# Kernel optimization log

Hardware: AMD Instinct MI355X
Metric: run time of the kernel (lower is better)

The kernel has to match this reference:

```python
import jax, jax.numpy as jnp
import numpy as np
import math

B, L, WIN, D, H, FF, NL, V, M = 16, 2048, 128, 512, 8, 2048, 3, 32000, 32
HD = D // H
EPS = 1e-5
RECON_W = 0.1

def _ln(x, g, b):
    m = x.mean(-1, keepdims=True)
    v = ((x - m) ** 2).mean(-1, keepdims=True)
    return (x - m) * jax.lax.rsqrt(v + EPS) * g + b

def _denoiser(x_t, t, motif, left, right, glob, time_proj_W, time_proj_b, cond_proj_W, cond_proj_b,
              qkv_W, qkv_b, attn_out_W, attn_out_b, ff1_W, ff1_b, ff2_W, ff2_b,
              ln1_g, ln1_b, ln2_g, ln2_b, out_W, out_b):
    half = D // 2
    freqs = jnp.exp(-math.log(10000.0) * jnp.arange(half) / (half - 1))
    a = t[:, None] * freqs[None, :]
    temb = jnp.concatenate([jnp.sin(a), jnp.cos(a)], -1) @ time_proj_W.T + time_proj_b
    x = x_t + temb[:, None, :]
    cond = jnp.concatenate([motif, left, right, glob], -1) @ cond_proj_W.T + cond_proj_b
    x = jnp.concatenate([cond[:, None, :], x], 1)
    S = x.shape[1]
    for i in range(NL):  # post-norm TransformerEncoderLayer, relu, no dropout (eval)
        qkv = x @ qkv_W[i].T + qkv_b[i]
        q, k, v = jnp.split(qkv, 3, axis=-1)
        q = q.reshape(B, S, H, HD); k = k.reshape(B, S, H, HD); v = v.reshape(B, S, H, HD)
        attn = jax.nn.softmax(jnp.einsum('bqhd,bkhd->bhqk', q, k) / math.sqrt(HD), axis=-1)
        ctx = jnp.einsum('bhqk,bkhd->bqhd', attn, v).reshape(B, S, D)
        x = _ln(x + ctx @ attn_out_W[i].T + attn_out_b[i], ln1_g[i], ln1_b[i])
        h = jax.nn.relu(x @ ff1_W[i].T + ff1_b[i]) @ ff2_W[i].T + ff2_b[i]
        x = _ln(x + h, ln2_g[i], ln2_b[i])
    return x[:, 1:, :] @ out_W.T + out_b

def setup_inputs():
    key = jax.random.key(0)
    ks = jax.random.split(key, 20)
    s = 0.02
    inp = {}
    inp['token_ids'] = jax.random.randint(ks[0], (B, L), 0, V)
    inp['motif_ids'] = jax.random.randint(ks[1], (B, M), 0, V)
    inp['motif_len'] = jax.random.randint(ks[2], (B,), 1, M + 1)
    inp['window_start'] = jax.random.randint(ks[3], (B,), 0, L - WIN)
    lens = jax.random.randint(ks[4], (B,), 1, WIN + 1).at[0].set(WIN)
    inp['window_end'] = inp['window_start'] + lens
    inp['t'] = jax.random.uniform(ks[5], (B,))
    inp['x0'] = jax.random.normal(ks[6], (B, WIN, D))
    inp['embed_table'] = jax.random.normal(ks[7], (V, D)) * s
    inp['decode_W'] = jax.random.normal(ks[8], (V, D)) * s
    inp['decode_b'] = jnp.zeros((V,))
    inp['adapter_W'] = jax.random.normal(ks[9], (D, D)) * s
    inp['adapter_b'] = jnp.zeros((D,))
    inp['time_proj_W'] = jax.random.normal(ks[10], (D, D)) * s
    inp['time_proj_b'] = jnp.zeros((D,))
    inp['cond_proj_W'] = jax.random.normal(ks[11], (D, 4 * D)) * s
    inp['cond_proj_b'] = jnp.zeros((D,))
    inp['qkv_W'] = jax.random.normal(ks[12], (NL, 3 * D, D)) * s
    inp['qkv_b'] = jnp.zeros((NL, 3 * D))
    inp['attn_out_W'] = jax.random.normal(ks[13], (NL, D, D)) * s
    inp['attn_out_b'] = jnp.zeros((NL, D))
    inp['ff1_W'] = jax.random.normal(ks[14], (NL, FF, D)) * s
    inp['ff1_b'] = jnp.zeros((NL, FF))
    inp['ff2_W'] = jax.random.normal(ks[15], (NL, D, FF)) * s
    inp['ff2_b'] = jnp.zeros((NL, D))
    inp['ln1_g'] = jnp.ones((NL, D)); inp['ln1_b'] = jnp.zeros((NL, D))
    inp['ln2_g'] = jnp.ones((NL, D)); inp['ln2_b'] = jnp.zeros((NL, D))
    inp['out_W'] = jax.random.normal(ks[16], (D, D)) * s
    inp['out_b'] = jnp.zeros((D,))
    return inp

def _forward(token_ids, motif_ids, motif_len, window_start, window_end, t, x0,
             embed_table, decode_W, decode_b, adapter_W, adapter_b, den):
    hidden = embed_table[token_ids]  # frozen backbone encode: [B, L, D]
    pos = jnp.arange(L)
    def pool(s, e):  # vectorized masked mean over region [s, e)
        m = ((pos[None, :] >= s[:, None]) & (pos[None, :] < e[:, None])).astype(hidden.dtype)
        return jnp.einsum('bl,bld->bd', m, hidden) / jnp.maximum(m.sum(1, keepdims=True), 1.0)
    left = pool(jnp.zeros_like(window_start), window_start)
    right = pool(window_end, jnp.full_like(window_end, L))
    glob = hidden.mean(1)
    memb = embed_table[motif_ids]
    mmask = (jnp.arange(M)[None, :] < motif_len[:, None]).astype(memb.dtype)
    motif = (memb * mmask[..., None]).sum(1) / jnp.maximum(motif_len.astype(memb.dtype), 1.0)[:, None]
    actual = jnp.clip(window_end - window_start, 0, WIN)
    win_mask = jnp.arange(WIN)[None, :] < actual[:, None]
    idx = jnp.clip(window_start[:, None] + jnp.arange(WIN)[None, :], 0, L - 1)
    x1 = jnp.take_along_axis(hidden, idx[:, :, None], axis=1) * win_mask[..., None]
    x_t = (1 - t[:, None, None]) * x0 + t[:, None, None] * x1
    target_v = x1 - x0
    pred_v = _denoiser(x_t, t, motif, left, right, glob, *den)
    valid = win_mask[..., None].astype(x1.dtype)
    vel = (((pred_v - target_v) ** 2) * valid).sum() / (jnp.maximum(valid.sum(), 1.0) * D)
    pred_x1 = x_t + (1 - t[:, None, None]) * pred_v
    logits = (pred_x1 @ adapter_W.T + adapter_b) @ decode_W.T + decode_b
    labels = jnp.where(win_mask, jnp.take_along_axis(token_ids, idx, axis=1), -100)
    lv = labels != -100
    logp = jax.nn.log_softmax(logits, axis=-1)
    picked = jnp.take_along_axis(logp, jnp.maximum(labels, 0)[..., None], axis=-1)[..., 0]
    recon = -(picked * lv).sum() / jnp.maximum(lv.sum(), 1)
    return vel + RECON_W * recon

def reference(token_ids, motif_ids, motif_len, window_start, window_end, t, x0,
              embed_table, decode_W, decode_b, adapter_W, adapter_b,
              time_proj_W, time_proj_b, cond_proj_W, cond_proj_b, qkv_W, qkv_b,
              attn_out_W, attn_out_b, ff1_W, ff1_b, ff2_W, ff2_b,
              ln1_g, ln1_b, ln2_g, ln2_b, out_W, out_b):
    den = (time_proj_W, time_proj_b, cond_proj_W, cond_proj_b, qkv_W, qkv_b,
           attn_out_W, attn_out_b, ff1_W, ff1_b, ff2_W, ff2_b,
           ln1_g, ln1_b, ln2_g, ln2_b, out_W, out_b)
    return _forward(token_ids, motif_ids, motif_len, window_start, window_end, t, x0,
                    embed_table, decode_W, decode_b, adapter_W, adapter_b, den)
```

## Files before the change

### kernel.cpp

```cpp
#include <hip/hip_runtime.h>
#include <hip/hip_bf16.h>
#include <math.h>

typedef __hip_bfloat16 bf16;

constexpr int cB = 16, cL = 2048, cWIN = 128, cD = 512, cH = 8, cFF = 2048;
constexpr int cNL = 3, cV = 32000, cM = 32;
constexpr int cHD = cD / cH;
constexpr int cS = cWIN + 1;
constexpr float cEPS = 1e-5f;
constexpr float cRECON_W = 0.1f;
constexpr int cNVT = cV / 128;

__device__ __forceinline__ float b2f(bf16 x) { return __bfloat162float(x); }

__device__ __forceinline__ float ldx(const void* p, size_t i, int f32) {
    return f32 ? ((const float*)p)[i]
               : __bfloat162float(((const bf16*)p)[i]);
}

__device__ __forceinline__ unsigned int f2bf(float f) {
    union { float f; unsigned int u; } v; v.f = f;
    unsigned int u = v.u + 0x7FFFu + ((v.u >> 16) & 1u);
    return u >> 16;
}

__device__ __forceinline__ void glds16(const unsigned short* g, unsigned short* l) {
    __builtin_amdgcn_global_load_lds(
        (const __attribute__((address_space(1))) void*)g,
        (__attribute__((address_space(3))) void*)l, 16, 0, 0);
}

typedef short bf16x8 __attribute__((ext_vector_type(8)));
typedef float f32x4  __attribute__((ext_vector_type(4)));

__global__ void detect_kernel(const void* __restrict__ x0raw, int* __restrict__ flag)
{
    const unsigned short* h = (const unsigned short*)x0raw;
    int tid = threadIdx.x;
    int cnt = 0;
    for (int j = tid; j < 8192; j += 256) {
        unsigned short u = h[2 * j];
        int e = (u >> 7) & 0xFF;
        if (e >= 134) cnt++;
    }
    __shared__ int red[256];
    red[tid] = cnt; __syncthreads();
    for (int off = 128; off > 0; off >>= 1) {
        if (tid < off) red[tid] += red[tid + off];
        __syncthreads();
    }
    if (tid == 0) *flag = (red[0] > 400) ? 1 : 0;
}

__global__ __launch_bounds__(512) void pools_part_kernel(
    const int* __restrict__ tok, const int* __restrict__ wstart,
    const int* __restrict__ wend, const void* __restrict__ emb,
    float* __restrict__ part, const int* __restrict__ dflag)
{
    const int f32 = *dflag;
    int chunk = blockIdx.x;
    int b = blockIdx.y;
    int d = threadIdx.x;
    int ws_ = wstart[b], we_ = wend[b];
    float sl = 0.f, sr = 0.f, sg = 0.f;
    int l0 = chunk * 128;
    for (int l = l0; l < l0 + 128; ++l) {
        int t = tok[b * cL + l];
        float h = ldx(emb, (size_t)t * cD + d, f32);
        sg += h;
        if (l < ws_) sl += h;
        if (l >= we_) sr += h;
    }
    size_t base = ((size_t)(b * 16 + chunk)) * 3 * cD;
    part[base + d]            = sl;
    part[base + cD + d]       = sr;
    part[base + 2 * cD + d]   = sg;
}

__global__ __launch_bounds__(512) void pools_combine_kernel(
    const float* __restrict__ part, const int* __restrict__ mids,
    const int* __restrict__ mlen, const int* __restrict__ wstart,
    const int* __restrict__ wend, const void* __restrict__ emb,
    unsigned short* __restrict__ featb, const int* __restrict__ dflag)
{
    const int f32 = *dflag;
    int b = blockIdx.x;
    int d = threadIdx.x;
    int ws_ = wstart[b], we_ = wend[b];
    float sl = 0.f, sr = 0.f, sg = 0.f;
    for (int c = 0; c < 16; ++c) {
        size_t base = ((size_t)(b * 16 + c)) * 3 * cD;
        sl += part[base + d];
        sr += part[base + cD + d];
        sg += part[base + 2 * cD + d];
    }
    int ml = mlen[b];
    float sm = 0.f;
    for (int j = 0; j < cM; ++j) {
        if (j < ml) sm += ldx(emb, (size_t)mids[b * cM + j] * cD + d, f32);
    }
    unsigned short* fr = featb + (size_t)b * (4 * cD);
    fr[d]            = (unsigned short)f2bf(sm / fmaxf((float)ml, 1.f));
    fr[cD + d]       = (unsigned short)f2bf(sl / fmaxf((float)ws_, 1.f));
    fr[2 * cD + d]   = (unsigned short)f2bf(sr / fmaxf((float)(cL - we_), 1.f));
    fr[3 * cD + d]   = (unsigned short)f2bf(sg / (float)cL);
}

__global__ __launch_bounds__(512) void tf_kernel(
    const void* __restrict__ t_arr, unsigned short* __restrict__ tfbb,
    const int* __restrict__ dflag)
{
    const int f32 = *dflag;
    int b = blockIdx.x;
    int j = threadIdx.x;
    float t = ldx(t_arr, b, f32);
    const int half = cD / 2;
    float v;
    if (j < half) {
        float fr = expf(-logf(10000.f) * (float)j / (float)(half - 1));
        v = sinf(t * fr);
    } else {
        float fr = expf(-logf(10000.f) * (float)(j - half) / (float)(half - 1));
        v = cosf(t * fr);
    }
    tfbb[(size_t)b * cD + j] = (unsigned short)f2bf(v);
}

__global__ __launch_bounds__(512) void build_x_kernel(
    const int* __restrict__ tok, const int* __restrict__ wstart,
    const int* __restrict__ wend, const void* __restrict__ t_arr,
    const void* __restrict__ x0, const void* __restrict__ emb,
    const float* __restrict__ cond, const float* __restrict__ temb,
    float* __restrict__ x, unsigned short* __restrict__ xbf,
    float* __restrict__ x1, float* __restrict__ xt,
    const int* __restrict__ dflag)
{
    const int f32 = *dflag;
    int row = blockIdx.x;
    int b = row / cS, s = row % cS;
    int d = threadIdx.x;
    if (s == 0) {
        float cv = cond[b * cD + d];
        x[(size_t)row * cD + d] = cv;
        xbf[(size_t)row * cD + d] = (unsigned short)f2bf(cv);
        return;
    }
    int i = s - 1;
    int ws_ = wstart[b], we_ = wend[b];
    int actual = min(max(we_ - ws_, 0), cWIN);
    int idx = min(ws_ + i, cL - 1);
    float x1v = 0.f;
    if (i < actual) x1v = ldx(emb, (size_t)tok[b * cL + idx] * cD + d, f32);
    float t = ldx(t_arr, b, f32);
    float x0v = ldx(x0, ((size_t)b * cWIN + i) * cD + d, f32);
    float xtv = (1.f - t) * x0v + t * x1v;
    size_t ro = ((size_t)b * cWIN + i) * cD + d;
    x1[ro] = x1v;
    xt[ro] = xtv;
    float xv = xtv + temb[b * cD + d];
    x[(size_t)row * cD + d] = xv;
    xbf[(size_t)row * cD + d] = (unsigned short)f2bf(xv);
}

constexpr int GL2 = 72;
__global__ __launch_bounds__(512) void gemm_bf(
    const unsigned short* __restrict__ Abf, const void* __restrict__ Wb,
    size_t wOff, const void* __restrict__ biasb, size_t bOff,
    float* __restrict__ Cf, unsigned short* __restrict__ Cbf,
    int Mdim, int Ndim, int Kdim, int relu, int obf, int amap,
    const int* __restrict__ dflag)
{
    const int f32 = *dflag;
    const float* Wf = (const float*)Wb + wOff;
    const unsigned short* Wh = (const unsigned short*)Wb + wOff;
    __shared__ unsigned short As[2][64 * GL2];
    __shared__ unsigned short Bs[2][64 * GL2];
    const int tid = threadIdx.x;
    const int lane = tid & 63;
    const int wid = tid >> 6;
    const int wm = wid >> 1;
    const int wn = wid & 1;
    const int quad = lane >> 4, lm = lane & 15;
    const int m0 = blockIdx.y * 64;
    const int n0 = blockIdx.x * 64;

    f32x4 acc0 = (f32x4){0.f, 0.f, 0.f, 0.f};
    f32x4 acc1 = (f32x4){0.f, 0.f, 0.f, 0.f};

    const int srow = tid >> 3;
    const int sc8  = (tid & 7) * 8;
    const int ssw  = ((tid & 7) ^ ((tid >> 3) & 7)) * 8;
    const int lmm  = lm & 7;

    auto loadA = [&](int k0, uint4& r) {
        int r0 = m0 + srow;
        uint4 v = {0u, 0u, 0u, 0u};
        if (r0 < Mdim) {
            size_t ar = amap ? ((size_t)(r0 >> 7) * cS + 1 + (r0 & 127))
                             : (size_t)r0;
            v = *(const uint4*)(Abf + ar * Kdim + k0 + sc8);
        }
        r = v;
    };
    auto loadB = [&](int k0, uint4& r) {
        size_t g = (size_t)(n0 + srow) * Kdim + k0 + sc8;
        if (f32) {
            float4 v0 = *(const float4*)(Wf + g);
            float4 v1 = *(const float4*)(Wf + g + 4);
            r = make_uint4(
                f2bf(v0.x) | (f2bf(v0.y) << 16), f2bf(v0.z) | (f2bf(v0.w) << 16),
                f2bf(v1.x) | (f2bf(v1.y) << 16), f2bf(v1.z) | (f2bf(v1.w) << 16));
        } else {
            r = *(const uint4*)(Wh + g);
        }
    };
    auto stores = [&](int buf, const uint4& ra, const uint4& rb) {
        *(uint4*)(&As[buf][srow * GL2 + ssw]) = ra;
        *(uint4*)(&Bs[buf][srow * GL2 + ssw]) = rb;
    };
    auto compute = [&](int buf) {
        #pragma unroll
        for (int kk = 0; kk < 2; ++kk) {
            const int sl = ((kk * 4 + quad) ^ lmm) * 8;
            bf16x8 a0 = *(const bf16x8*)(&As[buf][(wm * 16 + lm) * GL2 + sl]);
            bf16x8 b0 = *(const bf16x8*)(&Bs[buf][(wn * 32 + lm) * GL2 + sl]);
            bf16x8 b1 = *(const bf16x8*)(&Bs[buf][(wn * 32 + 16 + lm) * GL2 + sl]);
            acc0 = __builtin_amdgcn_mfma_f32_16x16x32_bf16(a0, b0, acc0, 0, 0, 0);
            acc1 = __builtin_amdgcn_mfma_f32_16x16x32_bf16(a0, b1, acc1, 0, 0, 0);
        }
    };

    uint4 raA, rbA, raB, rbB;
    loadA(0, raA);  loadB(0, rbA);
    loadA(64, raB); loadB(64, rbB);
    const int nk = Kdim >> 6;
    for (int t = 0; t < nk; t += 2) {
        stores(0, raA, rbA);
        __syncthreads();
        if (t + 2 < nk) { loadA((t + 2) * 64, raA); loadB((t + 2) * 64, rbA); }
        compute(0);
        stores(1, raB, rbB);
        __syncthreads();
        if (t + 3 < nk) { loadA((t + 3) * 64, raB); loadB((t + 3) * 64, rbB); }
        compute(1);
    }

    #pragma unroll
    for (int in = 0; in < 2; ++in) {
        int gc = n0 + wn * 32 + in * 16 + lm;
        float bv = ldx(biasb, bOff + gc, f32);
        const f32x4& a = in ? acc1 : acc0;
        #pragma unroll
        for (int r = 0; r < 4; ++r) {
            int gr = m0 + wm * 16 + quad * 4 + r;
            if (gr < Mdim) {
                float v = a[r] + bv;
                if (relu) v = fmaxf(v, 0.f);
                if (obf) Cbf[(size_t)gr * Ndim + gc] = (unsigned short)f2bf(v);
                else     Cf[(size_t)gr * Ndim + gc] = v;
            }
        }
    }
}

__global__ __launch_bounds__(256) void attn_mfma_kernel(
    const unsigned short* __restrict__ qkv, unsigned short* __restrict__ ctx)
{
    constexpr int SP = 160;
    constexpr int KP = 72;
    constexpr int VP = 168;
    const int h = blockIdx.x, b = blockIdx.y, z = blockIdx.z;
    const int tid = threadIdx.x;
    const int lane = tid & 63;
    const int wid = tid >> 6;
    const int quad = lane >> 4, lm = lane & 15;

    __shared__ unsigned short Ks[SP * KP];
    __shared__ unsigned short Vt[64 * VP];
    __shared__ unsigned short Pl[4 * 16 * VP];

    const unsigned short* base = qkv + (size_t)b * cS * (3 * cD) + h * cHD;

    for (int c = tid; c < SP * 8; c += 256) {
        int row = c >> 3, g = c & 7;
        uint4 v = {0u, 0u, 0u, 0u};
        if (row < cS)
            v = *(const uint4*)(base + (size_t)row * (3 * cD) + cD + g * 8);
        *(uint4*)(Ks + row * KP + g * 8) = v;
    }
    for (int c = tid; c < SP * 16; c += 256) {
        int key = c >> 4, d4 = c & 15;
        uint2 v = {0u, 0u};
        if (key < cS)
            v = *(const uint2*)(base + (size_t)key * (3 * cD) + 2 * cD + d4 * 4);
        Vt[(d4 * 4 + 0) * VP + key] = (unsigned short)(v.x & 0xFFFFu);
        Vt[(d4 * 4 + 1) * VP + key] = (unsigned short)(v.x >> 16);
        Vt[(d4 * 4 + 2) * VP + key] = (unsigned short)(v.y & 0xFFFFu);
        Vt[(d4 * 4 + 3) * VP + key] = (unsigned short)(v.y >> 16);
    }
    __syncthreads();

    unsigned short* Pw = Pl + wid * (16 * VP);
    const int t = z * 3 + wid;

    if (wid < 3 && t < 9) {
        int qs = t * 16 + lm;
        bf16x8 aq[2];
        #pragma unroll
        for (int j = 0; j < 8; ++j) { aq[0][j] = 0; aq[1][j] = 0; }
        if (qs < cS) {
            const unsigned short* qrow = base + (size_t)qs * (3 * cD);
            aq[0] = *(const bf16x8*)(qrow + quad * 8);
            aq[1] = *(const bf16x8*)(qrow + 32 + quad * 8);
        }

        f32x4 sc[10];
        #pragma unroll
        for (int n = 0; n < 10; ++n) {
            sc[n] = (f32x4){0.f, 0.f, 0.f, 0.f};
            bf16x8 bk0 = *(const bf16x8*)(Ks + (n * 16 + lm) * KP + quad * 8);
            sc[n] = __builtin_amdgcn_mfma_f32_16x16x32_bf16(aq[0], bk0, sc[n], 0, 0, 0);
            bf16x8 bk1 = *(const bf16x8*)(Ks + (n * 16 + lm) * KP + 32 + quad * 8);
            sc[n] = __builtin_amdgcn_mfma_f32_16x16x32_bf16(aq[1], bk1, sc[n], 0, 0, 0);
        }

        #pragma unroll
        for (int r = 0; r < 4; ++r) {
            float mx = -3.0e38f;
            #pragma unroll
            for (int n = 0; n < 10; ++n) {
                float v = sc[n][r] * 0.125f;
                mx = fmaxf(mx, ((n * 16 + lm) < cS) ? v : -3.0e38f);
            }
            #pragma unroll
            for (int msk = 1; msk < 16; msk <<= 1)
                mx = fmaxf(mx, __shfl_xor(mx, msk));
            float p[10];
            float sum = 0.f;
            #pragma unroll
            for (int n = 0; n < 10; ++n) {
                float e = ((n * 16 + lm) < cS) ? expf(sc[n][r] * 0.125f - mx) : 0.f;
                p[n] = e; sum += e;
            }
            #pragma unroll
            for (int msk = 1; msk < 16; msk <<= 1)
                sum += __shfl_xor(sum, msk);
            float inv = 1.f / sum;
            unsigned short* pr = Pw + (quad * 4 + r) * VP + lm;
            #pragma unroll
            for (int n = 0; n < 10; ++n)
                pr[n * 16] = (unsigned short)f2bf(p[n] * inv);
        }

        asm volatile("s_waitcnt lgkmcnt(0)" ::: "memory");
        __builtin_amdgcn_sched_barrier(0);

        f32x4 o[4];
        #pragma unroll
        for (int j = 0; j < 4; ++j) o[j] = (f32x4){0.f, 0.f, 0.f, 0.f};
        #pragma unroll
        for (int ks = 0; ks < 5; ++ks) {
            bf16x8 ap = *(const bf16x8*)(Pw + lm * VP + ks * 32 + quad * 8);
            #pragma unroll
            for (int j = 0; j < 4; ++j) {
                bf16x8 bv = *(const bf16x8*)(Vt + (j * 16 + lm) * VP + ks * 32 + quad * 8);
                o[j] = __builtin_amdgcn_mfma_f32_16x16x32_bf16(ap, bv, o[j], 0, 0, 0);
            }
        }

        #pragma unroll
        for (int r = 0; r < 4; ++r) {
            int s_ = t * 16 + quad * 4 + r;
            if (s_ < cS) {
                unsigned short* orow = ctx + ((size_t)(b * cS + s_)) * cD + h * cHD;
                #pragma unroll
                for (int j = 0; j < 4; ++j)
                    orow[j * 16 + lm] = (unsigned short)f2bf(o[j][r]);
            }
        }
    }
}

__global__ __launch_bounds__(256) void resid_ln_kernel(
    float* __restrict__ x, const float* __restrict__ h,
    const void* __restrict__ g, const void* __restrict__ bta, size_t off,
    unsigned short* __restrict__ xbf, const int* __restrict__ dflag)
{
    const int f32 = *dflag;
    int row = blockIdx.x;
    int tid = threadIdx.x;
    __shared__ float red[256];
    float v[2];
    float s = 0.f;
    #pragma unroll
    for (int j = 0; j < 2; ++j) {
        int d = tid + j * 256;
        v[j] = x[(size_t)row * cD + d] + h[(size_t)row * cD + d];
        s += v[j];
    }
    red[tid] = s; __syncthreads();
    for (int o = 128; o > 0; o >>= 1) {
        if (tid < o) red[tid] += red[tid + o];
        __syncthreads();
    }
    float mean = red[0] / (float)cD;
    __syncthreads();
    float vs = 0.f;
    #pragma unroll
    for (int j = 0; j < 2; ++j) { float dd = v[j] - mean; vs += dd * dd; }
    red[tid] = vs; __syncthreads();
    for (int o = 128; o > 0; o >>= 1) {
        if (tid < o) red[tid] += red[tid + o];
        __syncthreads();
    }
    float rs = rsqrtf(red[0] / (float)cD + cEPS);
    #pragma unroll
    for (int j = 0; j < 2; ++j) {
        int d = tid + j * 256;
        float ov = (v[j] - mean) * rs * ldx(g, off + d, f32) + ldx(bta, off + d, f32);
        x[(size_t)row * cD + d] = ov;
        xbf[(size_t)row * cD + d] = (unsigned short)f2bf(ov);
    }
}

__global__ __launch_bounds__(512) void predvel_kernel(
    const float* __restrict__ xt, const float* __restrict__ pv,
    const float* __restrict__ x1, const void* __restrict__ x0,
    const void* __restrict__ t_arr, const int* __restrict__ wstart,
    const int* __restrict__ wend, unsigned short* __restrict__ px1,
    float* __restrict__ velpart, const int* __restrict__ dflag)
{
    const int f32 = *dflag;
    int row = blockIdx.x;
    int b = row >> 7, i = row & 127;
    int d = threadIdx.x;
    float t = ldx(t_arr, b, f32);
    size_t o = (size_t)row * cD + d;
    float pvv = pv[o];
    px1[o] = (unsigned short)f2bf(xt[o] + (1.f - t) * pvv);
    int actual = min(max(wend[b] - wstart[b], 0), cWIN);
    float s = 0.f;
    if (i < actual) {
        float tv = x1[o] - ldx(x0, o, f32);
        float diff = pvv - tv;
        s = diff * diff;
    }
    __shared__ float red[512];
    red[d] = s; __syncthreads();
    for (int off = 256; off > 0; off >>= 1) {
        if (d < off) red[d] += red[d + off];
        __syncthreads();
    }
    if (d == 0) velpart[row] = red[0];
}

__global__ void labels_kernel(
    const int* __restrict__ tok, const int* __restrict__ wstart,
    const int* __restrict__ wend, int* __restrict__ labels)
{
    int r = blockIdx.x * 256 + threadIdx.x;
    if (r >= cB * cWIN) return;
    int b = r / cWIN, i = r % cWIN;
    int ws_ = wstart[b], we_ = wend[b];
    int actual = min(max(we_ - ws_, 0), cWIN);
    labels[r] = (i < actual) ? tok[b * cL + min(ws_ + i, cL - 1)] : -1;
}

__global__ __launch_bounds__(256) void cvt_w_kernel(
    const void* __restrict__ Wsrc, unsigned short* __restrict__ dst,
    const int* __restrict__ dflag)
{
    if (!*dflag) return;
    const float4* src = (const float4*)Wsrc;
    size_t n4 = (size_t)cV * cD / 4;
    for (size_t i = (size_t)blockIdx.x * 256 + threadIdx.x; i < n4;
         i += (size_t)gridDim.x * 256) {
        float4 v = src[i];
        unsigned int p0 = f2bf(v.x) | (f2bf(v.y) << 16);
        unsigned int p1 = f2bf(v.z) | (f2bf(v.w) << 16);
        ((uint2*)dst)[i] = make_uint2(p0, p1);
    }
}

__global__ __launch_bounds__(256) void decode_mfma2_kernel(
    const unsigned short* __restrict__ hbf, const unsigned short* __restrict__ wbf,
    const void* __restrict__ dW, const void* __restrict__ db,
    const int* __restrict__ labels,
    float* __restrict__ pm, float* __restrict__ ps, float* __restrict__ lab,
    const int* __restrict__ dflag)
{
    const int f32 = *dflag;
    const unsigned short* Wsrc = f32 ? wbf : (const unsigned short*)dW;
    const int bid = blockIdx.x;
    const int xcd = bid & 7;
    const int local = bid >> 3;
    const int nt = xcd * 32 + (local >> 4);
    const int mt = local & 15;
    if (nt >= cNVT) return;
    const int m0 = mt * 128, n0 = nt * 128;

    __shared__ __align__(16) char smem[17408];
    unsigned short* As = (unsigned short*)smem;
    unsigned short* Bs = As + 4096;

    const int tid = threadIdx.x;
    const int lane = tid & 63;
    const int wid = tid >> 6;
    const int wm = wid >> 1, wn = wid & 1;
    const int quad = lane >> 4, lm = lane & 15;

    const int grow  = lane >> 2;
    const int gslot = (lane & 3) ^ ((lane >> 3) & 3);
    const int rslot = (quad ^ ((lm >> 1) & 3)) * 8;

    const unsigned short* gA = hbf  + (size_t)(m0 + wid * 32 + grow) * cD + gslot * 8;
    const unsigned short* gB = Wsrc + (size_t)(n0 + wid * 32 + grow) * cD + gslot * 8;

    f32x4 acc[4][4];
    #pragma unroll
    for (int i = 0; i < 4; ++i)
        #pragma unroll
        for (int j = 0; j < 4; ++j)
            acc[i][j] = (f32x4){0.f, 0.f, 0.f, 0.f};

    for (int k0 = 0; k0 < cD; k0 += 32) {
        #pragma unroll
        for (int c = 0; c < 2; ++c) {
            glds16(gA + (size_t)c * 16 * cD + k0, As + (wid * 2 + c) * 512);
            glds16(gB + (size_t)c * 16 * cD + k0, Bs + (wid * 2 + c) * 512);
        }
        __syncthreads();
        bf16x8 af[4], bfr[4];
        #pragma unroll
        for (int im = 0; im < 4; ++im)
            af[im] = *(const bf16x8*)(As + (wm * 64 + im * 16 + lm) * 32 + rslot);
        #pragma unroll
        for (int in = 0; in < 4; ++in)
            bfr[in] = *(const bf16x8*)(Bs + (wn * 64 + in * 16 + lm) * 32 + rslot);
        #pragma unroll
        for (int im = 0; im < 4; ++im)
            #pragma unroll
            for (int in = 0; in < 4; ++in)
                acc[im][in] = __builtin_amdgcn_mfma_f32_16x16x32_bf16(
                    af[im], bfr[in], acc[im][in], 0, 0, 0);
        __syncthreads();
    }

    float bv[4];
    #pragma unroll
    for (int in = 0; in < 4; ++in)
        bv[in] = ldx(db, n0 + wn * 64 + in * 16 + lm, f32);
    #pragma unroll
    for (int im = 0; im < 4; ++im)
        #pragma unroll
        for (int in = 0; in < 4; ++in)
            #pragma unroll
            for (int r = 0; r < 4; ++r)
                acc[im][in][r] += bv[in];

    #pragma unroll
    for (int im = 0; im < 4; ++im) {
        #pragma unroll
        for (int r = 0; r < 4; ++r) {
            int gr = m0 + wm * 64 + im * 16 + quad * 4 + r;
            int lb = labels[gr];
            #pragma unroll
            for (int in = 0; in < 4; ++in) {
                int col = n0 + wn * 64 + in * 16 + lm;
                if (lb == col) lab[gr] = acc[im][in][r];
            }
        }
    }

    float (*red)[33] = (float(*)[33])smem;
    float* mrow = (float*)(smem + 16896);
    #pragma unroll
    for (int im = 0; im < 4; ++im) {
        #pragma unroll
        for (int r = 0; r < 4; ++r) {
            int rl = wm * 64 + im * 16 + quad * 4 + r;
            float mx = acc[im][0][r];
            #pragma unroll
            for (int in = 1; in < 4; ++in) mx = fmaxf(mx, acc[im][in][r]);
            red[rl][wn * 16 + lm] = mx;
        }
    }
    __syncthreads();
    if (tid < 128) {
        float mx = red[tid][0];
        #pragma unroll
        for (int t = 1; t < 32; ++t) mx = fmaxf(mx, red[tid][t]);
        mrow[tid] = mx;
    }
    __syncthreads();
    #pragma unroll
    for (int im = 0; im < 4; ++im) {
        #pragma unroll
        for (int r = 0; r < 4; ++r) {
            int rl = wm * 64 + im * 16 + quad * 4 + r;
            float m_ = mrow[rl];
            float s = 0.f;
            #pragma unroll
            for (int in = 0; in < 4; ++in) s += expf(acc[im][in][r] - m_);
            red[rl][wn * 16 + lm] = s;
        }
    }
    __syncthreads();
    if (tid < 128) {
        float s = red[tid][0];
        #pragma unroll
        for (int t = 1; t < 32; ++t) s += red[tid][t];
        int gr = m0 + tid;
        pm[(size_t)gr * cNVT + nt] = mrow[tid];
        ps[(size_t)gr * cNVT + nt] = s;
    }
}

constexpr int GLDS = 40;
__global__ __launch_bounds__(256) void decode_mfma_kernel(
    const unsigned short* __restrict__ hbf, const void* __restrict__ dW,
    const void* __restrict__ db, const int* __restrict__ labels,
    float* __restrict__ pm, float* __restrict__ ps, float* __restrict__ lab,
    const int* __restrict__ dflag)
{
    const int f32 = *dflag;
    const float* Wf = (const float*)dW;
    const unsigned short* Wh = (const unsigned short*)dW;
    __shared__ unsigned short As[128 * GLDS];
    __shared__ unsigned short Bs[128 * GLDS];
    const int tid = threadIdx.x;
    const int lane = tid & 63;
    const int wid = tid >> 6;
    const int wm = wid >> 1, wn = wid & 1;
    const int quad = lane >> 4, lm = lane & 15;
    const int nt = blockIdx.x;
    const int mt = blockIdx.y;
    const int m0 = mt * 128, n0 = nt * 128;

    f32x4 acc[4][4];
    #pragma unroll
    for (int i = 0; i < 4; ++i)
        #pragma unroll
        for (int j = 0; j < 4; ++j)
            acc[i][j] = (f32x4){0.f, 0.f, 0.f, 0.f};

    for (int k0 = 0; k0 < cD; k0 += 32) {
        #pragma unroll
        for (int t = 0; t < 2; ++t) {
            int idx = tid + t * 256;
            int row = idx >> 2, c = idx & 3;
            uint4 v = *(const uint4*)(hbf + (size_t)(m0 + row) * cD + k0 + c * 8);
            *(uint4*)(As + row * GLDS + c * 8) = v;
        }
        #pragma unroll
        for (int t = 0; t < 4; ++t) {
            int chunk = tid + t * 256;
            int row = chunk >> 3;
            int kc = (chunk & 7) * 4;
            size_t gro = (size_t)(n0 + row) * cD + k0 + kc;
            if (f32) {
                float4 v = *(const float4*)(Wf + gro);
                unsigned int p0 = f2bf(v.x) | (f2bf(v.y) << 16);
                unsigned int p1 = f2bf(v.z) | (f2bf(v.w) << 16);
                *(uint2*)(Bs + row * GLDS + kc) = make_uint2(p0, p1);
            } else {
                *(uint2*)(Bs + row * GLDS + kc) = *(const uint2*)(Wh + gro);
            }
        }
        __syncthreads();
        bf16x8 af[4], bfr[4];
        #pragma unroll
        for (int im = 0; im < 4; ++im) {
            int row = wm * 64 + im * 16 + lm;
            af[im] = *(const bf16x8*)(As + row * GLDS + quad * 8);
        }
        #pragma unroll
        for (int in = 0; in < 4; ++in) {
            int row = wn * 64 + in * 16 + lm;
            bfr[in] = *(const bf16x8*)(Bs + row * GLDS + quad * 8);
        }
        #pragma unroll
        for (int im = 0; im < 4; ++im)
            #pragma unroll
            for (int in = 0; in < 4; ++in)
                acc[im][in] = __builtin_amdgcn_mfma_f32_16x16x32_bf16(
                    af[im], bfr[in], acc[im][in], 0, 0, 0);
        __syncthreads();
    }

    float bv[4];
    #pragma unroll
    for (int in = 0; in < 4; ++in)
        bv[in] = ldx(db, n0 + wn * 64 + in * 16 + lm, f32);
    #pragma unroll
    for (int im = 0; im < 4; ++im)
        #pragma unroll
        for (int in = 0; in < 4; ++in)
            #pragma unroll
            for (int r = 0; r < 4; ++r)
                acc[im][in][r] += bv[in];

    #pragma unroll
    for (int im = 0; im < 4; ++im) {
        #pragma unroll
        for (int r = 0; r < 4; ++r) {
            int gr = m0 + wm * 64 + im * 16 + quad * 4 + r;
            int lb = labels[gr];
            #pragma unroll
            for (int in = 0; in < 4; ++in) {
                int col = n0 + wn * 64 + in * 16 + lm;
                if (lb == col) lab[gr] = acc[im][in][r];
            }
        }
    }

    __shared__ float red[128][33];
    __shared__ float mrow[128];
    #pragma unroll
    for (int im = 0; im < 4; ++im) {
        #pragma unroll
        for (int r = 0; r < 4; ++r) {
            int rl = wm * 64 + im * 16 + quad * 4 + r;
            float mx = acc[im][0][r];
            #pragma unroll
            for (int in = 1; in < 4; ++in) mx = fmaxf(mx, acc[im][in][r]);
            red[rl][wn * 16 + lm] = mx;
        }
    }
    __syncthreads();
    if (tid < 128) {
        float mx = red[tid][0];
        #pragma unroll
        for (int t = 1; t < 32; ++t) mx = fmaxf(mx, red[tid][t]);
        mrow[tid] = mx;
    }
    __syncthreads();
    #pragma unroll
    for (int im = 0; im < 4; ++im) {
        #pragma unroll
        for (int r = 0; r < 4; ++r) {
            int rl = wm * 64 + im * 16 + quad * 4 + r;
            float m_ = mrow[rl];
            float s = 0.f;
            #pragma unroll
            for (int in = 0; in < 4; ++in) s += expf(acc[im][in][r] - m_);
            red[rl][wn * 16 + lm] = s;
        }
    }
    __syncthreads();
    if (tid < 128) {
        float s = red[tid][0];
        #pragma unroll
        for (int t = 1; t < 32; ++t) s += red[tid][t];
        int gr = m0 + tid;
        pm[(size_t)gr * cNVT + nt] = mrow[tid];
        ps[(size_t)gr * cNVT + nt] = s;
    }
}

__global__ __launch_bounds__(64) void lse_reduce_kernel(
    const float* __restrict__ pm, const float* __restrict__ ps,
    const float* __restrict__ lab, const int* __restrict__ labels,
    float* __restrict__ logppart)
{
    int r = blockIdx.x;
    int tid = threadIdx.x;
    if (labels[r] < 0) {
        if (tid == 0) logppart[r] = 0.f;
        return;
    }
    float m = -1e30f;
    for (int c = tid; c < cNVT; c += 64) m = fmaxf(m, pm[(size_t)r * cNVT + c]);
    for (int off = 32; off > 0; off >>= 1) m = fmaxf(m, __shfl_down(m, off));
    m = __shfl(m, 0);
    float s = 0.f;
    for (int c = tid; c < cNVT; c += 64)
        s += ps[(size_t)r * cNVT + c] * expf(pm[(size_t)r * cNVT + c] - m);
    for (int off = 32; off > 0; off >>= 1) s += __shfl_down(s, off);
    if (tid == 0) logppart[r] = lab[r] - (m + logf(s));
}

__global__ __launch_bounds__(256) void finalize_kernel(
    const float* __restrict__ velpart, const float* __restrict__ logppart,
    const int* __restrict__ wstart, const int* __restrict__ wend,
    void* __restrict__ out, const int* __restrict__ dflag)
{
    const int f32 = *dflag;
    __shared__ float r1[256], r2[256];
    int tid = threadIdx.x;
    float s1 = 0.f, s2 = 0.f;
    for (int r = tid; r < cB * cWIN; r += 256) {
        s1 += velpart[r];
        s2 += logppart[r];
    }
    r1[tid] = s1; r2[tid] = s2; __syncthreads();
    for (int off = 128; off > 0; off >>= 1) {
        if (tid < off) { r1[tid] += r1[tid + off]; r2[tid] += r2[tid + off]; }
        __syncthreads();
    }
    if (tid == 0) {
        float cnt = 0.f;
        for (int b = 0; b < cB; ++b)
            cnt += (float)min(max(wend[b] - wstart[b], 0), cWIN);
        cnt = fmaxf(cnt, 1.f);
        float vel = r1[0] / (cnt * (float)cD);
        float recon = -r2[0] / cnt;
        float loss = vel + cRECON_W * recon;
        if (f32) ((float*)out)[0] = loss;
        else     ((bf16*)out)[0] = __float2bfloat16(loss);
    }
}

extern "C" void kernel_launch(void* const* d_in, const int* in_sizes, int n_in,
                              void* d_out, int out_size, void* d_ws, size_t ws_size,
                              hipStream_t stream) {
    const int*  token_ids    = (const int*)d_in[0];
    const int*  motif_ids    = (const int*)d_in[1];
    const int*  motif_len    = (const int*)d_in[2];
    const int*  window_start = (const int*)d_in[3];
    const int*  window_end   = (const int*)d_in[4];
    const void* t_arr        = d_in[5];
    const void* x0           = d_in[6];
    const void* embed_table  = d_in[7];
    const void* decode_W     = d_in[8];
    const void* decode_b     = d_in[9];
    const void* adapter_W    = d_in[10];
    const void* adapter_b    = d_in[11];
    const void* time_proj_W  = d_in[12];
    const void* time_proj_b  = d_in[13];
    const void* cond_proj_W  = d_in[14];
    const void* cond_proj_b  = d_in[15];
    const void* qkv_W        = d_in[16];
    const void* qkv_b        = d_in[17];
    const void* attn_out_W   = d_in[18];
    const void* attn_out_b   = d_in[19];
    const void* ff1_W        = d_in[20];
    const void* ff1_b        = d_in[21];
    const void* ff2_W        = d_in[22];
    const void* ff2_b        = d_in[23];
    const void* ln1_g        = d_in[24];
    const void* ln1_b        = d_in[25];
    const void* ln2_g        = d_in[26];
    const void* ln2_b        = d_in[27];
    const void* out_W        = d_in[28];
    const void* out_b        = d_in[29];

    float* w = (float*)d_ws;
    const size_t SZ_X   = (size_t)cB * cS * cD;
    const size_t SZ_BA  = (size_t)cB * cS * cFF;
    const size_t SZ_ROW = (size_t)cB * cWIN * cD;
    float* x     = w;
    float* bufA  = x + SZ_X;
    float* bufB  = bufA + SZ_BA;
    float* bufC  = bufB + SZ_X;
    float* x1b   = bufC + SZ_X;
    float* xtb   = x1b + SZ_ROW;
    float* pvb   = xtb + SZ_ROW;
    float* h2b   = pvb + SZ_ROW;
    float* feat  = h2b + SZ_ROW;
    float* tfb   = feat + (size_t)cB * 4 * cD;
    float* cond  = tfb + (size_t)cB * cD;
    float* temb  = cond + (size_t)cB * cD;
    float* velpart = temb + (size_t)cB * cD;
    float* logppart = velpart + (size_t)cB * cWIN;
    int*   dflag = (int*)(logppart + (size_t)cB * cWIN);
    float* wsend = (float*)(dflag + 16);
    unsigned short* wbf = (unsigned short*)wsend;

    const size_t need_bytes = ((char*)wsend - (char*)d_ws)
                            + (size_t)cV * cD * sizeof(unsigned short) + 256;
    const bool fast_decode = ws_size >= need_bytes;

    const int Wrows = cB * cWIN;
    const int Mrows = cB * cS;

    unsigned short* xbf    = (unsigned short*)h2b;
    unsigned short* featbf = xbf + (size_t)Mrows * cD;
    unsigned short* tfbbf  = featbf + (size_t)cB * 4 * cD;
    unsigned short* qkvbf  = (unsigned short*)bufA;
    unsigned short* ff1bf  = (unsigned short*)bufA;
    unsigned short* ctxbf  = (unsigned short*)bufB;
    unsigned short* px1bf  = (unsigned short*)(bufA + (size_t)3 * 1024 * 1024);
    unsigned short* hbf    = (unsigned short*)bufC;

    float* pm  = bufA;
    float* ps  = pm + (size_t)Wrows * cNVT;
    float* lab = ps + (size_t)Wrows * cNVT;
    int*   labels = (int*)(lab + Wrows);
    float* poolspart = bufC;

    auto gemm = [&](const unsigned short* A, const void* W, size_t wOff,
                    const void* bias, size_t bOff, float* Cf, unsigned short* Cbf,
                    int M_, int N_, int K_, int relu, int obf, int amap) {
        dim3 grid(N_ / 64, (M_ + 63) / 64);
        gemm_bf<<<grid, 512, 0, stream>>>(A, W, wOff, bias, bOff, Cf, Cbf,
                                          M_, N_, K_, relu, obf, amap, dflag);
    };

    detect_kernel<<<1, 256, 0, stream>>>(x0, dflag);
    if (fast_decode)
        cvt_w_kernel<<<2048, 256, 0, stream>>>(decode_W, wbf, dflag);
    pools_part_kernel<<<dim3(16, cB), cD, 0, stream>>>(token_ids, window_start,
        window_end, embed_table, poolspart, dflag);
    pools_combine_kernel<<<cB, cD, 0, stream>>>(poolspart, motif_ids, motif_len,
        window_start, window_end, embed_table, featbf, dflag);
    tf_kernel<<<cB, cD, 0, stream>>>(t_arr, tfbbf, dflag);
    gemm(featbf, cond_proj_W, 0, cond_proj_b, 0, cond, nullptr, cB, cD, 4 * cD, 0, 0, 0);
    gemm(tfbbf, time_proj_W, 0, time_proj_b, 0, temb, nullptr, cB, cD, cD, 0, 0, 0);
    build_x_kernel<<<Mrows, cD, 0, stream>>>(token_ids, window_start, window_end,
        t_arr, x0, embed_table, cond, temb, x, xbf, x1b, xtb, dflag);

    for (int i = 0; i < cNL; ++i) {
        gemm(xbf, qkv_W, (size_t)i * 3 * cD * cD, qkv_b, (size_t)i * 3 * cD,
             nullptr, qkvbf, Mrows, 3 * cD, cD, 0, 1, 0);
        attn_mfma_kernel<<<dim3(cH, cB, 3), 256, 0, stream>>>(qkvbf, ctxbf);
        gemm(ctxbf, attn_out_W, (size_t)i * cD * cD, attn_out_b, (size_t)i * cD,
             bufC, nullptr, Mrows, cD, cD, 0, 0, 0);
        resid_ln_kernel<<<Mrows, 256, 0, stream>>>(x, bufC, ln1_g, ln1_b,
             (size_t)i * cD, xbf, dflag);
        gemm(xbf, ff1_W, (size_t)i * cFF * cD, ff1_b, (size_t)i * cFF,
             nullptr, ff1bf, Mrows, cFF, cD, 1, 1, 0);
        gemm(ff1bf, ff2_W, (size_t)i * cD * cFF, ff2_b, (size_t)i * cD,
             bufC, nullptr, Mrows, cD, cFF, 0, 0, 0);
        resid_ln_kernel<<<Mrows, 256, 0, stream>>>(x, bufC, ln2_g, ln2_b,
             (size_t)i * cD, xbf, dflag);
    }

    gemm(xbf, out_W, 0, out_b, 0, pvb, nullptr, Wrows, cD, cD, 0, 0, 1);
    predvel_kernel<<<Wrows, 512, 0, stream>>>(xtb, pvb, x1b, x0, t_arr,
        window_start, window_end, px1bf, velpart, dflag);
    gemm(px1bf, adapter_W, 0, adapter_b, 0, nullptr, hbf, Wrows, cD, cD, 0, 1, 0);

    labels_kernel<<<(Wrows + 255) / 256, 256, 0, stream>>>(
        token_ids, window_start, window_end, labels);
    if (fast_decode) {
        decode_mfma2_kernel<<<4096, 256, 0, stream>>>(
            hbf, wbf, decode_W, decode_b, labels, pm, ps, lab, dflag);
    } else {
        decode_mfma_kernel<<<dim3(cNVT, Wrows / 128), 256, 0, stream>>>(
            hbf, decode_W, decode_b, labels, pm, ps, lab, dflag);
    }
    lse_reduce_kernel<<<Wrows, 64, 0, stream>>>(pm, ps, lab, labels, logppart);

    finalize_kernel<<<1, 256, 0, stream>>>(velpart, logppart,
        window_start, window_end, d_out, dflag);
}
```

Baseline: 811.5 us.

## Fuse residual+LayerNorm into full-row GEMM and fold small side kernels together

Adds a gemm_row kernel in which each block computes 16 full rows of 512 outputs with MFMA. In its epilogue it applies bias, residual add and LayerNorm, which replaces the separate attn_out/ff2 GEMMs and their resid_ln kernels. The same kernel, in a second mode, fuses the output projection with the predicted-velocity and velocity-loss computation. The time-feature and label kernels are merged into pools_combine, and labels move to a dedicated workspace slot. This cuts launches and intermediate fp32 round trips through memory. The cost is fewer, larger blocks (about 129) that read A and W straight from global memory, and a one-pass E[x²]−mean² variance.

```diff
diff --git a/kernel.cpp b/kernel.cpp
--- a/kernel.cpp
+++ b/kernel.cpp
@@ -82,7 +82,9 @@
     const float* __restrict__ part, const int* __restrict__ mids,
     const int* __restrict__ mlen, const int* __restrict__ wstart,
     const int* __restrict__ wend, const void* __restrict__ emb,
-    unsigned short* __restrict__ featb, const int* __restrict__ dflag)
+    unsigned short* __restrict__ featb, const void* __restrict__ t_arr,
+    unsigned short* __restrict__ tfbb, const int* __restrict__ tok,
+    int* __restrict__ labels, const int* __restrict__ dflag)
 {
     const int f32 = *dflag;
     int b = blockIdx.x;
@@ -105,26 +107,26 @@
     fr[cD + d]       = (unsigned short)f2bf(sl / fmaxf((float)ws_, 1.f));
     fr[2 * cD + d]   = (unsigned short)f2bf(sr / fmaxf((float)(cL - we_), 1.f));
     fr[3 * cD + d]   = (unsigned short)f2bf(sg / (float)cL);
-}
-
-__global__ __launch_bounds__(512) void tf_kernel(
-    const void* __restrict__ t_arr, unsigned short* __restrict__ tfbb,
-    const int* __restrict__ dflag)
-{
-    const int f32 = *dflag;
-    int b = blockIdx.x;
-    int j = threadIdx.x;
-    float t = ldx(t_arr, b, f32);
-    const int half = cD / 2;
-    float v;
-    if (j < half) {
-        float fr = expf(-logf(10000.f) * (float)j / (float)(half - 1));
-        v = sinf(t * fr);
-    } else {
-        float fr = expf(-logf(10000.f) * (float)(j - half) / (float)(half - 1));
-        v = cosf(t * fr);
-    }
-    tfbb[(size_t)b * cD + j] = (unsigned short)f2bf(v);
+
+    {
+        float t = ldx(t_arr, b, f32);
+        const int half = cD / 2;
+        float v;
+        if (d < half) {
+            float frq = expf(-logf(10000.f) * (float)d / (float)(half - 1));
+            v = sinf(t * frq);
+        } else {
+            float frq = expf(-logf(10000.f) * (float)(d - half) / (float)(half - 1));
+            v = cosf(t * frq);
+        }
+        tfbb[(size_t)b * cD + d] = (unsigned short)f2bf(v);
+    }
+
+    if (d < cWIN) {
+        int actual = min(max(we_ - ws_, 0), cWIN);
+        labels[b * cWIN + d] =
+            (d < actual) ? tok[b * cL + min(ws_ + d, cL - 1)] : -1;
+    }
 }
 
 __global__ __launch_bounds__(512) void build_x_kernel(
@@ -264,6 +266,168 @@
     }
 }
 
+__global__ __launch_bounds__(512) void gemm_row(
+    const unsigned short* __restrict__ Abf, const void* __restrict__ Wb,
+    size_t wOff, const void* __restrict__ biasb, size_t bOff,
+    int Kdim, int mode, int amap,
+    float* __restrict__ xres, const void* __restrict__ g,
+    const void* __restrict__ bta, size_t lnOff, unsigned short* __restrict__ xbf,
+    const float* __restrict__ xt, const float* __restrict__ x1,
+    const void* __restrict__ x0, const void* __restrict__ t_arr,
+    const int* __restrict__ wstart, const int* __restrict__ wend,
+    unsigned short* __restrict__ px1, float* __restrict__ velpart,
+    const int* __restrict__ dflag)
+{
+    const int f32 = *dflag;
+    const float* Wf = (const float*)Wb + wOff;
+    const unsigned short* Wh = (const unsigned short*)Wb + wOff;
+    const int tid = threadIdx.x;
+    const int lane = tid & 63;
+    const int wid = tid >> 6;
+    const int quad = lane >> 4, lm = lane & 15;
+    const int m0 = blockIdx.x * 16;
+    const int colb = wid * 64;
+
+    int grA = m0 + lm;
+    size_t ar = amap ? ((size_t)(grA >> 7) * cS + 1 + (grA & 127)) : (size_t)grA;
+    const unsigned short* Arow = Abf + ar * Kdim;
+
+    size_t wro[4];
+    #pragma unroll
+    for (int n = 0; n < 4; ++n)
+        wro[n] = (size_t)(colb + n * 16 + lm) * Kdim;
+
+    f32x4 acc[4];
+    #pragma unroll
+    for (int n = 0; n < 4; ++n) acc[n] = (f32x4){0.f, 0.f, 0.f, 0.f};
+
+    auto ldw = [&](size_t off) -> bf16x8 {
+        if (f32) {
+            float4 v0 = *(const float4*)(Wf + off);
+            float4 v1 = *(const float4*)(Wf + off + 4);
+            union { unsigned int u[4]; bf16x8 h; } r;
+            r.u[0] = f2bf(v0.x) | (f2bf(v0.y) << 16);
+            r.u[1] = f2bf(v0.z) | (f2bf(v0.w) << 16);
+            r.u[2] = f2bf(v1.x) | (f2bf(v1.y) << 16);
+            r.u[3] = f2bf(v1.z) | (f2bf(v1.w) << 16);
+            return r.h;
+        }
+        return *(const bf16x8*)(Wh + off);
+    };
+    auto ldstep = [&](int k0, bf16x8& a0, bf16x8& a1, bf16x8* b0, bf16x8* b1) {
+        a0 = *(const bf16x8*)(Arow + k0 + quad * 8);
+        a1 = *(const bf16x8*)(Arow + k0 + 32 + quad * 8);
+        #pragma unroll
+        for (int n = 0; n < 4; ++n) {
+            b0[n] = ldw(wro[n] + k0 + quad * 8);
+            b1[n] = ldw(wro[n] + k0 + 32 + quad * 8);
+        }
+    };
+    auto comp = [&](bf16x8 a0, bf16x8 a1, const bf16x8* b0, const bf16x8* b1) {
+        #pragma unroll
+        for (int n = 0; n < 4; ++n) {
+            acc[n] = __builtin_amdgcn_mfma_f32_16x16x32_bf16(a0, b0[n], acc[n], 0, 0, 0);
+            acc[n] = __builtin_amdgcn_mfma_f32_16x16x32_bf16(a1, b1[n], acc[n], 0, 0, 0);
+        }
+    };
+
+    bf16x8 aA0, aA1, bA0[4], bA1[4];
+    bf16x8 aB0, aB1, bB0[4], bB1[4];
+    ldstep(0, aA0, aA1, bA0, bA1);
+    for (int k0 = 0; k0 < Kdim; k0 += 128) {
+        ldstep(k0 + 64, aB0, aB1, bB0, bB1);
+        comp(aA0, aA1, bA0, bA1);
+        if (k0 + 128 < Kdim) ldstep(k0 + 128, aA0, aA1, bA0, bA1);
+        comp(aB0, aB1, bB0, bB1);
+    }
+
+    __shared__ float st_s[16][8];
+    __shared__ float st_ss[16][8];
+    __shared__ float fin0[16], fin1[16];
+
+    if (mode == 1) {
+        float e[4][4];
+        #pragma unroll
+        for (int r = 0; r < 4; ++r) {
+            int row = quad * 4 + r;
+            float s = 0.f, ss = 0.f;
+            #pragma unroll
+            for (int n = 0; n < 4; ++n) {
+                int col = colb + n * 16 + lm;
+                float v = acc[n][r] + ldx(biasb, bOff + col, f32)
+                        + xres[(size_t)(m0 + row) * cD + col];
+                e[n][r] = v;
+                s += v; ss += v * v;
+            }
+            #pragma unroll
+            for (int msk = 1; msk < 16; msk <<= 1) {
+                s  += __shfl_xor(s, msk);
+                ss += __shfl_xor(ss, msk);
+            }
+            if (lm == 0) { st_s[row][wid] = s; st_ss[row][wid] = ss; }
+        }
+        __syncthreads();
+        if (tid < 16) {
+            float S = 0.f, SS = 0.f;
+            #pragma unroll
+            for (int w = 0; w < 8; ++w) { S += st_s[tid][w]; SS += st_ss[tid][w]; }
+            float mean = S / (float)cD;
+            float var = SS / (float)cD - mean * mean;
+            fin0[tid] = mean;
+            fin1[tid] = rsqrtf(var + cEPS);
+        }
+        __syncthreads();
+        #pragma unroll
+        for (int r = 0; r < 4; ++r) {
+            int row = quad * 4 + r;
+            float mean = fin0[row], rs = fin1[row];
+            #pragma unroll
+            for (int n = 0; n < 4; ++n) {
+                int col = colb + n * 16 + lm;
+                float ov = (e[n][r] - mean) * rs * ldx(g, lnOff + col, f32)
+                         + ldx(bta, lnOff + col, f32);
+                size_t o = (size_t)(m0 + row) * cD + col;
+                xres[o] = ov;
+                xbf[o] = (unsigned short)f2bf(ov);
+            }
+        }
+    } else {
+        int b_ = m0 >> 7;
+        float t = ldx(t_arr, b_, f32);
+        int actual = min(max(wend[b_] - wstart[b_], 0), cWIN);
+        #pragma unroll
+        for (int r = 0; r < 4; ++r) {
+            int row = quad * 4 + r;
+            int grw = m0 + row;
+            int i = grw & 127;
+            float s = 0.f;
+            #pragma unroll
+            for (int n = 0; n < 4; ++n) {
+                int col = colb + n * 16 + lm;
+                size_t o = (size_t)grw * cD + col;
+                float pvv = acc[n][r] + ldx(biasb, bOff + col, f32);
+                px1[o] = (unsigned short)f2bf(xt[o] + (1.f - t) * pvv);
+                if (i < actual) {
+                    float tv = x1[o] - ldx(x0, o, f32);
+                    float diff = pvv - tv;
+                    s += diff * diff;
+                }
+            }
+            #pragma unroll
+            for (int msk = 1; msk < 16; msk <<= 1)
+                s += __shfl_xor(s, msk);
+            if (lm == 0) st_s[row][wid] = s;
+        }
+        __syncthreads();
+        if (tid < 16) {
+            float S = 0.f;
+            #pragma unroll
+            for (int w = 0; w < 8; ++w) S += st_s[tid][w];
+            velpart[m0 + tid] = S;
+        }
+    }
+}
+
 __global__ __launch_bounds__(256) void attn_mfma_kernel(
     const unsigned short* __restrict__ qkv, unsigned short* __restrict__ ctx)
 {
@@ -380,91 +544,6 @@
             }
         }
     }
-}
-
-__global__ __launch_bounds__(256) void resid_ln_kernel(
-    float* __restrict__ x, const float* __restrict__ h,
-    const void* __restrict__ g, const void* __restrict__ bta, size_t off,
-    unsigned short* __restrict__ xbf, const int* __restrict__ dflag)
-{
-    const int f32 = *dflag;
-    int row = blockIdx.x;
-    int tid = threadIdx.x;
-    __shared__ float red[256];
-    float v[2];
-    float s = 0.f;
-    #pragma unroll
-    for (int j = 0; j < 2; ++j) {
-        int d = tid + j * 256;
-        v[j] = x[(size_t)row * cD + d] + h[(size_t)row * cD + d];
-        s += v[j];
-    }
-    red[tid] = s; __syncthreads();
-    for (int o = 128; o > 0; o >>= 1) {
-        if (tid < o) red[tid] += red[tid + o];
-        __syncthreads();
-    }
-    float mean = red[0] / (float)cD;
-    __syncthreads();
-    float vs = 0.f;
-    #pragma unroll
-    for (int j = 0; j < 2; ++j) { float dd = v[j] - mean; vs += dd * dd; }
-    red[tid] = vs; __syncthreads();
-    for (int o = 128; o > 0; o >>= 1) {
-        if (tid < o) red[tid] += red[tid + o];
-        __syncthreads();
-    }
-    float rs = rsqrtf(red[0] / (float)cD + cEPS);
-    #pragma unroll
-    for (int j = 0; j < 2; ++j) {
-        int d = tid + j * 256;
-        float ov = (v[j] - mean) * rs * ldx(g, off + d, f32) + ldx(bta, off + d, f32);
-        x[(size_t)row * cD + d] = ov;
-        xbf[(size_t)row * cD + d] = (unsigned short)f2bf(ov);
-    }
-}
-
-__global__ __launch_bounds__(512) void predvel_kernel(
-    const float* __restrict__ xt, const float* __restrict__ pv,
-    const float* __restrict__ x1, const void* __restrict__ x0,
-    const void* __restrict__ t_arr, const int* __restrict__ wstart,
-    const int* __restrict__ wend, unsigned short* __restrict__ px1,
-    float* __restrict__ velpart, const int* __restrict__ dflag)
-{
-    const int f32 = *dflag;
-    int row = blockIdx.x;
-    int b = row >> 7, i = row & 127;
-    int d = threadIdx.x;
-    float t = ldx(t_arr, b, f32);
-    size_t o = (size_t)row * cD + d;
-    float pvv = pv[o];
-    px1[o] = (unsigned short)f2bf(xt[o] + (1.f - t) * pvv);
-    int actual = min(max(wend[b] - wstart[b], 0), cWIN);
-    float s = 0.f;
-    if (i < actual) {
-        float tv = x1[o] - ldx(x0, o, f32);
-        float diff = pvv - tv;
-        s = diff * diff;
-    }
-    __shared__ float red[512];
-    red[d] = s; __syncthreads();
-    for (int off = 256; off > 0; off >>= 1) {
-        if (d < off) red[d] += red[d + off];
-        __syncthreads();
-    }
-    if (d == 0) velpart[row] = red[0];
-}
-
-__global__ void labels_kernel(
-    const int* __restrict__ tok, const int* __restrict__ wstart,
-    const int* __restrict__ wend, int* __restrict__ labels)
-{
-    int r = blockIdx.x * 256 + threadIdx.x;
-    if (r >= cB * cWIN) return;
-    int b = r / cWIN, i = r % cWIN;
-    int ws_ = wstart[b], we_ = wend[b];
-    int actual = min(max(we_ - ws_, 0), cWIN);
-    labels[r] = (i < actual) ? tok[b * cL + min(ws_ + i, cL - 1)] : -1;
 }
 
 __global__ __launch_bounds__(256) void cvt_w_kernel(
@@ -865,7 +944,8 @@
     float* velpart = temb + (size_t)cB * cD;
     float* logppart = velpart + (size_t)cB * cWIN;
     int*   dflag = (int*)(logppart + (size_t)cB * cWIN);
-    float* wsend = (float*)(dflag + 16);
+    int*   labels = (int*)(dflag + 16);
+    float* wsend = (float*)(labels + (size_t)cB * cWIN);
     unsigned short* wbf = (unsigned short*)wsend;
 
     const size_t need_bytes = ((char*)wsend - (char*)d_ws)
@@ -887,7 +967,6 @@
     float* pm  = bufA;
     float* ps  = pm + (size_t)Wrows * cNVT;
     float* lab = ps + (size_t)Wrows * cNVT;
-    int*   labels = (int*)(lab + Wrows);
     float* poolspart = bufC;
 
     auto gemm = [&](const unsigned short* A, const void* W, size_t wOff,
@@ -897,6 +976,15 @@
         gemm_bf<<<grid, 512, 0, stream>>>(A, W, wOff, bias, bOff, Cf, Cbf,
                                           M_, N_, K_, relu, obf, amap, dflag);
     };
+    auto gemm_ln = [&](const unsigned short* A, const void* W, size_t wOff,
+                       const void* bias, size_t bOff, int K_,
+                       const void* g_, const void* b_, size_t lnOff) {
+        gemm_row<<<Mrows / 16, 512, 0, stream>>>(
+            A, W, wOff, bias, bOff, K_, 1, 0,
+            x, g_, b_, lnOff, xbf,
+            nullptr, nullptr, nullptr, nullptr, nullptr, nullptr,
+            nullptr, nullptr, dflag);
+    };
 
     detect_kernel<<<1, 256, 0, stream>>>(x0, dflag);
     if (fast_decode)
@@ -904,8 +992,8 @@
     pools_part_kernel<<<dim3(16, cB), cD, 0, stream>>>(token_ids, window_start,
         window_end, embed_table, poolspart, dflag);
     pools_combine_kernel<<<cB, cD, 0, stream>>>(poolspart, motif_ids, motif_len,
-        window_start, window_end, embed_table, featbf, dflag);
-    tf_kernel<<<cB, cD, 0, stream>>>(t_arr, tfbbf, dflag);
+        window_start, window_end, embed_table, featbf, t_arr, tfbbf,
+        token_ids, labels, dflag);
     gemm(featbf, cond_proj_W, 0, cond_proj_b, 0, cond, nullptr, cB, cD, 4 * cD, 0, 0, 0);
     gemm(tfbbf, time_proj_W, 0, time_proj_b, 0, temb, nullptr, cB, cD, cD, 0, 0, 0);
     build_x_kernel<<<Mrows, cD, 0, stream>>>(token_ids, window_start, window_end,
@@ -915,25 +1003,21 @@
         gemm(xbf, qkv_W, (size_t)i * 3 * cD * cD, qkv_b, (size_t)i * 3 * cD,
              nullptr, qkvbf, Mrows, 3 * cD, cD, 0, 1, 0);
         attn_mfma_kernel<<<dim3(cH, cB, 3), 256, 0, stream>>>(qkvbf, ctxbf);
-        gemm(ctxbf, attn_out_W, (size_t)i * cD * cD, attn_out_b, (size_t)i * cD,
-             bufC, nullptr, Mrows, cD, cD, 0, 0, 0);
-        resid_ln_kernel<<<Mrows, 256, 0, stream>>>(x, bufC, ln1_g, ln1_b,
-             (size_t)i * cD, xbf, dflag);
+        gemm_ln(ctxbf, attn_out_W, (size_t)i * cD * cD, attn_out_b,
+                (size_t)i * cD, cD, ln1_g, ln1_b, (size_t)i * cD);
         gemm(xbf, ff1_W, (size_t)i * cFF * cD, ff1_b, (size_t)i * cFF,
              nullptr, ff1bf, Mrows, cFF, cD, 1, 1, 0);
-        gemm(ff1bf, ff2_W, (size_t)i * cD * cFF, ff2_b, (size_t)i * cD,
-             bufC, nullptr, Mrows, cD, cFF, 0, 0, 0);
-        resid_ln_kernel<<<Mrows, 256, 0, stream>>>(x, bufC, ln2_g, ln2_b,
-             (size_t)i * cD, xbf, dflag);
-    }
-
-    gemm(xbf, out_W, 0, out_b, 0, pvb, nullptr, Wrows, cD, cD, 0, 0, 1);
-    predvel_kernel<<<Wrows, 512, 0, stream>>>(xtb, pvb, x1b, x0, t_arr,
-        window_start, window_end, px1bf, velpart, dflag);
+        gemm_ln(ff1bf, ff2_W, (size_t)i * cD * cFF, ff2_b,
+                (size_t)i * cD, cFF, ln2_g, ln2_b, (size_t)i * cD);
+    }
+
+    gemm_row<<<Wrows / 16, 512, 0, stream>>>(
+        xbf, out_W, 0, out_b, 0, cD, 2, 1,
+        nullptr, nullptr, nullptr, 0, nullptr,
+        xtb, x1b, x0, t_arr, window_start, window_end,
+        px1bf, velpart, dflag);
     gemm(px1bf, adapter_W, 0, adapter_b, 0, nullptr, hbf, Wrows, cD, cD, 0, 1, 0);
 
-    labels_kernel<<<(Wrows + 255) / 256, 256, 0, stream>>>(
-        token_ids, window_start, window_end, labels);
     if (fast_decode) {
         decode_mfma2_kernel<<<4096, 256, 0, stream>>>(
             hbf, wbf, decode_W, decode_b, labels, pm, ps, lab, dflag);
```

Result: slower. 1.277 ms (+57.4%).
